# Kernel tuning notes

Hardware: AMD Instinct MI355X
Metric: run time of the kernel (lower is better)

## Reference

```python
import jax, jax.numpy as jnp
import numpy as np

B, T, D_MODEL, N_HEAD, D_C = 2, 2048, 2048, 16, 512
D_HEAD = D_MODEL // N_HEAD          # 128
D_ROPE = D_C // N_HEAD              # 32 (rope projections are split into heads too)


def setup_inputs() -> dict:
    key = jax.random.key(0)
    ks = jax.random.split(key, 16)
    s = 0.02
    # weights stored as [in, out] (transpose of torch Linear.weight)
    return {
        "x":     jax.random.normal(ks[0], (B, T, D_MODEL), jnp.float32),
        "W_DKV": jax.random.normal(ks[1], (D_MODEL, D_C), jnp.float32) * s,
        "b_DKV": jnp.zeros((D_C,), jnp.float32),
        "W_UK":  jax.random.normal(ks[2], (D_C, D_MODEL), jnp.float32) * s,
        "b_UK":  jnp.zeros((D_MODEL,), jnp.float32),
        "W_UV":  jax.random.normal(ks[3], (D_C, D_MODEL), jnp.float32) * s,
        "b_UV":  jnp.zeros((D_MODEL,), jnp.float32),
        "W_DQ":  jax.random.normal(ks[4], (D_MODEL, D_C), jnp.float32) * s,
        "b_DQ":  jnp.zeros((D_C,), jnp.float32),
        "W_UQ":  jax.random.normal(ks[5], (D_C, D_MODEL), jnp.float32) * s,
        "b_UQ":  jnp.zeros((D_MODEL,), jnp.float32),
        "W_QR":  jax.random.normal(ks[6], (D_C, D_C), jnp.float32) * s,
        "b_QR":  jnp.zeros((D_C,), jnp.float32),
        "W_KR":  jax.random.normal(ks[7], (D_MODEL, D_C), jnp.float32) * s,
        "b_KR":  jnp.zeros((D_C,), jnp.float32),
    }


def _rope(x):
    # x: [B, H, T, d]; matches torch RoPE: split-even/odd then concat halves
    t, d = x.shape[2], x.shape[-1]
    freqs = 10000.0 ** (-(jnp.arange(0, d, 2, dtype=jnp.float32) / d))  # [d/2]
    theta = jnp.arange(t, dtype=jnp.float32)[:, None] * freqs[None, :]  # [T, d/2]
    cos, sin = jnp.cos(theta), jnp.sin(theta)
    x1, x2 = x[..., ::2], x[..., 1::2]
    return jnp.concatenate([x1 * cos - x2 * sin, x1 * sin + x2 * cos], axis=-1)


def _heads(x):
    b, t, _ = x.shape
    return x.reshape(b, t, N_HEAD, -1).transpose(0, 2, 1, 3)  # [B,H,T,dh]


def reference(x, W_DKV, b_DKV, W_UK, b_UK, W_UV, b_UV, W_DQ, b_DQ,
              W_UQ, b_UQ, W_QR, b_QR, W_KR, b_KR):
    b, t, _ = x.shape
    c_kv = x @ W_DKV + b_DKV                 # [B,T,d_c]
    k_content = _heads(c_kv @ W_UK + b_UK)   # [B,H,T,d_head]
    v = _heads(c_kv @ W_UV + b_UV)           # [B,H,T,d_head]
    c_q = x @ W_DQ + b_DQ
    q_content = _heads(c_q @ W_UQ + b_UQ)    # [B,H,T,d_head]
    q_rope = _rope(_heads(c_q @ W_QR + b_QR))  # [B,H,T,d_rope]
    k_rope = _rope(_heads(x @ W_KR + b_KR))    # [B,H,T,d_rope]
    Q = jnp.concatenate([q_content, q_rope], axis=-1)  # [B,H,T,d_head+d_rope]
    K = jnp.concatenate([k_content, k_rope], axis=-1)
    scale = 1.0 / jnp.sqrt(jnp.float32(Q.shape[-1]))
    scores = jnp.einsum("bhqd,bhkd->bhqk", Q, K) * scale
    probs = jax.nn.softmax(scores, axis=-1)
    out = jnp.einsum("bhqk,bhkd->bhqd", probs, v)
    return out.transpose(0, 2, 1, 3).reshape(b, t, -1)
```

## Files before the change

kernel.cpp:

```cpp
#include <hip/hip_runtime.h>
#include <hip/hip_bf16.h>
#include <cstdint>
#include <cstddef>

typedef __attribute__((ext_vector_type(8)))  short bf16x8;
typedef __attribute__((ext_vector_type(4)))  float f32x4;
typedef __attribute__((ext_vector_type(16))) float f32x16;
typedef __attribute__((ext_vector_type(4)))  int   i32x4;

#define DEVINL __device__ __forceinline__

#define ATT_SCALE 0.07905694150420949f
#define QSCALE    (0.07905694150420949f * 1.4426950408889634f)

DEVINL unsigned short f2bf(float f) {
  unsigned int u = __float_as_uint(f);
  u += 0x7fff + ((u >> 16) & 1);
  return (unsigned short)(u >> 16);
}

DEVINL int cvtpk(float lo, float hi) {
  int r;
  asm("v_cvt_pk_bf16_f32 %0, %1, %2" : "=v"(r) : "v"(lo), "v"(hi));
  return r;
}

DEVINL void stage16(const unsigned short* __restrict__ g, unsigned short* lds_u, int lane) {
  (void)lane;
  __builtin_amdgcn_global_load_lds((const __attribute__((address_space(1))) void*)g,
                                   (__attribute__((address_space(3))) void*)lds_u, 16, 0, 0);
}

__global__ void k_cvt_x(const float* __restrict__ x, unsigned short* __restrict__ o, int n) {
  int i = (blockIdx.x * blockDim.x + threadIdx.x) * 4;
  if (i >= n) return;
  float4 v = *reinterpret_cast<const float4*>(x + i);
  ushort4 r;
  r.x = f2bf(v.x); r.y = f2bf(v.y); r.z = f2bf(v.z); r.w = f2bf(v.w);
  *reinterpret_cast<ushort4*>(o + i) = r;
}

struct TwArgs { const float* W[7]; unsigned short* D[7]; };
__global__ void k_tw_all(TwArgs a) {
  __shared__ float t[32][33];
  const int bid = blockIdx.x;
  int w, K, N, bx, by;
  if (bid < 3072)      { w = bid >> 10; int r = bid & 1023; K = 2048; N = 512;  bx = r & 15; by = r >> 4; }
  else if (bid < 6144) { int r = bid - 3072; w = 3 + (r >> 10); r &= 1023; K = 512; N = 2048; bx = r & 63; by = r >> 6; }
  else                 { int r = bid - 6144; w = 6; K = 512; N = 512; bx = r & 15; by = r >> 4; }
  const float* W = a.W[w];
  unsigned short* D = a.D[w];
  const int n0 = bx * 32, k0 = by * 32;
  const int tx = threadIdx.x, ty = threadIdx.y;
#pragma unroll
  for (int j = 0; j < 4; j++)
    t[ty + j * 8][tx] = W[(size_t)(k0 + ty + j * 8) * N + n0 + tx];
  __syncthreads();
#pragma unroll
  for (int j = 0; j < 4; j++)
    D[(size_t)(n0 + ty + j * 8) * K + k0 + tx] = f2bf(t[tx][ty + j * 8]);
}

DEVINL size_t koff(int bh, int t, int d) {
  const int it = t >> 6, t6 = t & 63;
  const int kvt = t6 >> 5, lanelo = t6 & 31;
  const int ks = d >> 4, hi = (d >> 3) & 1, e = d & 7;
  return ((size_t)bh * 32 + it) * 10240 + (size_t)(kvt * 10 + ks) * 512 + (hi * 32 + lanelo) * 8 + e;
}
DEVINL size_t voff(int bh, int t, int dv) {
  const int it = t >> 6, t6 = t & 63;
  const int ks = t6 >> 4, hi = (t6 >> 3) & 1, e = t6 & 7;
  const int dvt = dv >> 5, lanelo = dv & 31;
  return ((size_t)bh * 32 + it) * 8192 + (size_t)(dvt * 4 + ks) * 512 + (hi * 32 + lanelo) * 8 + e;
}

__global__ __launch_bounds__(256) void k_gemm1(const unsigned short* __restrict__ A,
                                               const unsigned short* __restrict__ BT,
                                               const float* __restrict__ bias0,
                                               const float* __restrict__ bias1,
                                               const float* __restrict__ bias2,
                                               unsigned short* __restrict__ o0,
                                               unsigned short* __restrict__ o1,
                                               float* __restrict__ o2) {
  __shared__ unsigned short sA[128 * 64];
  __shared__ unsigned short sB[128 * 64];
  const int K = 2048;
  const int tid = threadIdx.x;
  const int lane = tid & 63, wid = tid >> 6;
  const int wr = wid >> 1, wc = wid & 1;
  const int row0 = blockIdx.y * 128, col0 = blockIdx.x * 128;
  const int lc = lane & 15, lg = lane >> 4;
  const int srow = lane >> 3, scol = (lane & 7) * 8;

  f32x4 acc[4][4];
#pragma unroll
  for (int m = 0; m < 4; m++)
#pragma unroll
    for (int n = 0; n < 4; n++) acc[m][n] = f32x4{0.f, 0.f, 0.f, 0.f};

  for (int k0 = 0; k0 < K; k0 += 64) {
#pragma unroll
    for (int i = 0; i < 4; i++) {
      const int chunk = wid * 4 + i;
      const int r = chunk * 8 + srow;
      stage16(A + (size_t)(row0 + r) * K + k0 + scol, sA + chunk * 512, lane);
      stage16(BT + (size_t)(col0 + r) * K + k0 + scol, sB + chunk * 512, lane);
    }
    asm volatile("s_waitcnt vmcnt(0)" ::: "memory");
    __syncthreads();
#pragma unroll
    for (int ks = 0; ks < 2; ks++) {
      bf16x8 af[4], bfr[4];
#pragma unroll
      for (int m = 0; m < 4; m++)
        af[m] = *reinterpret_cast<const bf16x8*>(sA + (wr * 64 + m * 16 + lc) * 64 + ks * 32 + lg * 8);
#pragma unroll
      for (int n = 0; n < 4; n++)
        bfr[n] = *reinterpret_cast<const bf16x8*>(sB + (wc * 64 + n * 16 + lc) * 64 + ks * 32 + lg * 8);
#pragma unroll
      for (int m = 0; m < 4; m++)
#pragma unroll
        for (int n = 0; n < 4; n++)
          acc[m][n] = __builtin_amdgcn_mfma_f32_16x16x32_bf16(af[m], bfr[n], acc[m][n], 0, 0, 0);
    }
    __syncthreads();
  }

  const int lr = lg * 4;
#pragma unroll
  for (int m = 0; m < 4; m++)
#pragma unroll
    for (int n = 0; n < 4; n++) {
      const int col = col0 + wc * 64 + n * 16 + lc;
      const float bv = (col < 512) ? bias0[col] : (col < 1024) ? bias1[col - 512] : bias2[col - 1024];
#pragma unroll
      for (int r = 0; r < 4; r++) {
        const int row = row0 + wr * 64 + m * 16 + lr + r;
        const float v = acc[m][n][r] + bv;
        if (col < 512)        o0[(size_t)row * 512 + col] = f2bf(v);
        else if (col < 1024)  o1[(size_t)row * 512 + col - 512] = f2bf(v);
        else                  o2[(size_t)row * 512 + col - 1024] = v;
      }
    }
}

__global__ __launch_bounds__(256) void k_gemm2(const unsigned short* __restrict__ ckv,
                                               const unsigned short* __restrict__ cq,
                                               const unsigned short* __restrict__ WT2,
                                               const unsigned short* __restrict__ WT3,
                                               const float* __restrict__ bUK,
                                               const float* __restrict__ bUV,
                                               const float* __restrict__ bUQ,
                                               const float* __restrict__ bQR,
                                               unsigned short* __restrict__ Kfb,
                                               unsigned short* __restrict__ Vfb,
                                               unsigned short* __restrict__ Qbuf,
                                               float* __restrict__ qrp) {
  __shared__ unsigned short sA[128 * 64];
  __shared__ unsigned short sB[128 * 64];
  const int K = 512;
  const bool m11 = blockIdx.x < 32;
  const unsigned short* A  = m11 ? ckv : cq;
  const unsigned short* BT = m11 ? WT2 : WT3;
  const int tid = threadIdx.x;
  const int lane = tid & 63, wid = tid >> 6;
  const int wr = wid >> 1, wc = wid & 1;
  const int row0 = blockIdx.y * 128;
  const int col0 = (m11 ? blockIdx.x : (blockIdx.x - 32)) * 128;
  const int lc = lane & 15, lg = lane >> 4;
  const int srow = lane >> 3, scol = (lane & 7) * 8;

  f32x4 acc[4][4];
#pragma unroll
  for (int m = 0; m < 4; m++)
#pragma unroll
    for (int n = 0; n < 4; n++) acc[m][n] = f32x4{0.f, 0.f, 0.f, 0.f};

  for (int k0 = 0; k0 < K; k0 += 64) {
#pragma unroll
    for (int i = 0; i < 4; i++) {
      const int chunk = wid * 4 + i;
      const int r = chunk * 8 + srow;
      stage16(A + (size_t)(row0 + r) * K + k0 + scol, sA + chunk * 512, lane);
      stage16(BT + (size_t)(col0 + r) * K + k0 + scol, sB + chunk * 512, lane);
    }
    asm volatile("s_waitcnt vmcnt(0)" ::: "memory");
    __syncthreads();
#pragma unroll
    for (int ks = 0; ks < 2; ks++) {
      bf16x8 af[4], bfr[4];
#pragma unroll
      for (int m = 0; m < 4; m++)
        af[m] = *reinterpret_cast<const bf16x8*>(sA + (wr * 64 + m * 16 + lc) * 64 + ks * 32 + lg * 8);
#pragma unroll
      for (int n = 0; n < 4; n++)
        bfr[n] = *reinterpret_cast<const bf16x8*>(sB + (wc * 64 + n * 16 + lc) * 64 + ks * 32 + lg * 8);
#pragma unroll
      for (int m = 0; m < 4; m++)
#pragma unroll
        for (int n = 0; n < 4; n++)
          acc[m][n] = __builtin_amdgcn_mfma_f32_16x16x32_bf16(af[m], bfr[n], acc[m][n], 0, 0, 0);
    }
    __syncthreads();
  }

  const int lr = lg * 4;
#pragma unroll
  for (int m = 0; m < 4; m++)
#pragma unroll
    for (int n = 0; n < 4; n++) {
      const int col = col0 + wc * 64 + n * 16 + lc;
      float bv;
      if (m11) bv = (col < 2048) ? bUK[col] : bUV[col - 2048];
      else     bv = (col < 2048) ? bUQ[col] : bQR[col - 2048];
#pragma unroll
      for (int r = 0; r < 4; r++) {
        const int row = row0 + wr * 64 + m * 16 + lr + r;
        const float v = acc[m][n][r] + bv;
        const int b = row >> 11, t = row & 2047;
        if (m11) {
          if (col < 2048) {
            const int h = col >> 7, d = col & 127;
            Kfb[koff(b * 16 + h, t, d)] = f2bf(v);
          } else {
            const int c = col - 2048, h = c >> 7, dv = c & 127;
            Vfb[voff(b * 16 + h, t, dv)] = f2bf(v);
          }
        } else {
          if (col < 2048) {
            const int h = col >> 7, d = col & 127;
            Qbuf[((size_t)(b * 16 + h) * 2048 + t) * 160 + d] = f2bf(v * QSCALE);
          } else {
            qrp[(size_t)row * 512 + col - 2048] = v;
          }
        }
      }
    }
}

__global__ void k_rope(const float* __restrict__ qpre, const float* __restrict__ kpre,
                       unsigned short* __restrict__ Qb, unsigned short* __restrict__ Kf) {
  const int idx = blockIdx.x * blockDim.x + threadIdx.x;
  const int which = idx >> 20;
  const int e = idx & 1048575;
  const int i = e & 15, h = (e >> 4) & 15, row = e >> 8;
  const int t = row & 2047, b = row >> 11;
  const float* pre = which ? kpre : qpre;
  const float x1 = pre[(size_t)row * 512 + h * 32 + 2 * i];
  const float x2 = pre[(size_t)row * 512 + h * 32 + 2 * i + 1];
  const float f = exp2f(-(float)i * (13.287712379549449f / 16.f));
  const float th = (float)t * f;
  float sv, cv;
  sincosf(th, &sv, &cv);
  const float o1 = x1 * cv - x2 * sv, o2 = x1 * sv + x2 * cv;
  if (which == 0) {
    const size_t base = ((size_t)(b * 16 + h) * 2048 + t) * 160 + 128;
    Qb[base + i]      = f2bf(o1 * QSCALE);
    Qb[base + 16 + i] = f2bf(o2 * QSCALE);
  } else {
    Kf[koff(b * 16 + h, t, 128 + i)] = f2bf(o1);
    Kf[koff(b * 16 + h, t, 144 + i)] = f2bf(o2);
  }
}

DEVINL float vmax32(const f32x16& a, const f32x16& b) {
  float t[16];
#pragma unroll
  for (int j = 0; j < 16; j++) t[j] = fmaxf(a[j], b[j]);
#pragma unroll
  for (int s = 8; s >= 1; s >>= 1)
#pragma unroll
    for (int j = 0; j < s; j++) t[j] = fmaxf(t[j], t[j + s]);
  return t[0];
}

DEVINL void loadV(const unsigned short* __restrict__ Vt, bf16x8 v[16], int lane) {
#pragma unroll
  for (int f = 0; f < 16; f++)
    v[f] = *reinterpret_cast<const bf16x8*>(Vt + (size_t)f * 512 + lane * 8);
}

DEVINL void subiter(const unsigned short* __restrict__ sKb, const bf16x8 qf[10],
                    const bf16x8 vfr[16], f32x16 o[4], float& mrun, float& lrun,
                    int lane, int hi) {
  f32x16 s0 = {}, s1 = {};
  __builtin_amdgcn_s_setprio(1);
#pragma unroll
  for (int ks = 0; ks < 10; ks++) {
    bf16x8 kf0 = *reinterpret_cast<const bf16x8*>(sKb + (size_t)ks * 512 + lane * 8);
    s0 = __builtin_amdgcn_mfma_f32_32x32x16_bf16(kf0, qf[ks], s0, 0, 0, 0);
    bf16x8 kf1 = *reinterpret_cast<const bf16x8*>(sKb + (size_t)(10 + ks) * 512 + lane * 8);
    s1 = __builtin_amdgcn_mfma_f32_32x32x16_bf16(kf1, qf[ks], s1, 0, 0, 0);
  }
  __builtin_amdgcn_s_setprio(0);

  float mx = vmax32(s0, s1);
  mx = fmaxf(mx, __shfl_xor(mx, 32));

  if (__any(mx > mrun + 8.f)) {
    const float mn = fmaxf(mrun, mx);
    const float corr = exp2f(mrun - mn);
    lrun *= corr;
#pragma unroll
    for (int d = 0; d < 4; d++)
#pragma unroll
      for (int r = 0; r < 16; r++) o[d][r] *= corr;
    mrun = mn;
  }

  float pe0[16], pe1[16];
#pragma unroll
  for (int r = 0; r < 16; r++) pe0[r] = exp2f(s0[r] - mrun);
#pragma unroll
  for (int r = 0; r < 16; r++) pe1[r] = exp2f(s1[r] - mrun);
  float a[16];
#pragma unroll
  for (int j = 0; j < 8; j++) {
    a[j]     = pe0[2 * j] + pe0[2 * j + 1];
    a[8 + j] = pe1[2 * j] + pe1[2 * j + 1];
  }
#pragma unroll
  for (int s = 8; s >= 1; s >>= 1)
#pragma unroll
    for (int j = 0; j < s; j++) a[j] += a[j + s];
  float rs = a[0];
  rs += __shfl_xor(rs, 32);
  lrun += rs;

  int W0[8], W1[8], S0w[8], S1w[8];
#pragma unroll
  for (int j = 0; j < 8; j++) {
    W0[j] = cvtpk(pe0[2 * j], pe0[2 * j + 1]);
    W1[j] = cvtpk(pe1[2 * j], pe1[2 * j + 1]);
  }
#pragma unroll
  for (int j = 0; j < 8; j++) {
    S0w[j] = __shfl_xor(W0[j], 32);
    S1w[j] = __shfl_xor(W1[j], 32);
  }
  bf16x8 pa[4];
  {
    i32x4 w0 = hi ? i32x4{S0w[2], S0w[3], W0[2], W0[3]} : i32x4{W0[0], W0[1], S0w[0], S0w[1]};
    i32x4 w1 = hi ? i32x4{S0w[6], S0w[7], W0[6], W0[7]} : i32x4{W0[4], W0[5], S0w[4], S0w[5]};
    i32x4 w2 = hi ? i32x4{S1w[2], S1w[3], W1[2], W1[3]} : i32x4{W1[0], W1[1], S1w[0], S1w[1]};
    i32x4 w3 = hi ? i32x4{S1w[6], S1w[7], W1[6], W1[7]} : i32x4{W1[4], W1[5], S1w[4], S1w[5]};
    pa[0] = __builtin_bit_cast(bf16x8, w0);
    pa[1] = __builtin_bit_cast(bf16x8, w1);
    pa[2] = __builtin_bit_cast(bf16x8, w2);
    pa[3] = __builtin_bit_cast(bf16x8, w3);
  }

  __builtin_amdgcn_s_setprio(1);
#pragma unroll
  for (int ks = 0; ks < 4; ks++) {
    o[0] = __builtin_amdgcn_mfma_f32_32x32x16_bf16(vfr[ks],      pa[ks], o[0], 0, 0, 0);
    o[1] = __builtin_amdgcn_mfma_f32_32x32x16_bf16(vfr[4 + ks],  pa[ks], o[1], 0, 0, 0);
    o[2] = __builtin_amdgcn_mfma_f32_32x32x16_bf16(vfr[8 + ks],  pa[ks], o[2], 0, 0, 0);
    o[3] = __builtin_amdgcn_mfma_f32_32x32x16_bf16(vfr[12 + ks], pa[ks], o[3], 0, 0, 0);
  }
  __builtin_amdgcn_s_setprio(0);
}

__global__ __launch_bounds__(256, 2) void k_attn(const unsigned short* __restrict__ Qb,
                                                 const unsigned short* __restrict__ Kf,
                                                 const unsigned short* __restrict__ Vf,
                                                 float* __restrict__ out) {
  __shared__ unsigned short sK[4][10240];
  const int lane = threadIdx.x & 63, wid = threadIdx.x >> 6;
  const int lanelo = lane & 31, hi = lane >> 5;

  const int L = blockIdx.x;
  const int xcd = L & 7, w = L >> 3;
  const int bh = xcd * 4 + (w & 3);
  const int qblk = w >> 2;
  const int b = bh >> 4, h = bh & 15;
  const int q0 = qblk * 128 + wid * 32;

  const unsigned short* Qh = Qb + (size_t)bh * 2048 * 160;
  const unsigned short* Kh = Kf + (size_t)bh * 32 * 10240;
  const unsigned short* Vh = Vf + (size_t)bh * 32 * 8192;

  bf16x8 qf[10];
#pragma unroll
  for (int ks = 0; ks < 10; ks++)
    qf[ks] = *reinterpret_cast<const bf16x8*>(Qh + (size_t)(q0 + lanelo) * 160 + ks * 16 + hi * 8);

#pragma unroll
  for (int i = 0; i < 10; i++) {
    const int chunk = wid * 10 + i;
    stage16(Kh + (size_t)chunk * 512 + lane * 8, &sK[0][0] + chunk * 512, lane);
  }

  f32x16 o[4] = {};
  float mrun = -1e30f, lrun = 0.f;

  asm volatile("s_waitcnt vmcnt(0)" ::: "memory");
  __syncthreads();

  for (int p = 0; p < 16; p++) {
    const int base = (p & 1) * 2;
    bf16x8 vA[16];
    loadV(Vh + (size_t)(2 * p) * 8192, vA, lane);
    if (p < 15) {
      const unsigned short* src = Kh + (size_t)(2 * p + 2) * 10240;
      unsigned short* dst = &sK[base ^ 2][0];
#pragma unroll
      for (int i = 0; i < 10; i++) {
        const int chunk = wid * 10 + i;
        stage16(src + (size_t)chunk * 512 + lane * 8, dst + chunk * 512, lane);
      }
    }
    subiter(&sK[base][0], qf, vA, o, mrun, lrun, lane, hi);
    bf16x8 vB[16];
    loadV(Vh + (size_t)(2 * p + 1) * 8192, vB, lane);
    subiter(&sK[base + 1][0], qf, vB, o, mrun, lrun, lane, hi);

    asm volatile("s_waitcnt vmcnt(0)" ::: "memory");
    __syncthreads();
  }

  const float inv = 1.f / lrun;
  float* sO = reinterpret_cast<float*>(&sK[0][0]) + wid * 1152;
#pragma unroll
  for (int dvt = 0; dvt < 4; dvt++) {
    __syncthreads();
#pragma unroll
    for (int r = 0; r < 16; r++) {
      const int dvl = (r & 3) + 8 * (r >> 2) + 4 * hi;
      sO[lanelo * 36 + dvl] = o[dvt][r] * inv;
    }
    __syncthreads();
#pragma unroll
    for (int p = 0; p < 4; p++) {
      const int q = p * 8 + (lane >> 3), c = (lane & 7) * 4;
      float4 v = *reinterpret_cast<const float4*>(sO + q * 36 + c);
      *reinterpret_cast<float4*>(out + ((size_t)b * 2048 + q0 + q) * 2048 + h * 128 + dvt * 32 + c) = v;
    }
  }
}

extern "C" void kernel_launch(void* const* d_in, const int* in_sizes, int n_in,
                              void* d_out, int out_size, void* d_ws, size_t ws_size,
                              hipStream_t stream) {
  (void)in_sizes; (void)n_in; (void)out_size;
  const float* x     = (const float*)d_in[0];
  const float* W_DKV = (const float*)d_in[1];
  const float* b_DKV = (const float*)d_in[2];
  const float* W_UK  = (const float*)d_in[3];
  const float* b_UK  = (const float*)d_in[4];
  const float* W_UV  = (const float*)d_in[5];
  const float* b_UV  = (const float*)d_in[6];
  const float* W_DQ  = (const float*)d_in[7];
  const float* b_DQ  = (const float*)d_in[8];
  const float* W_UQ  = (const float*)d_in[9];
  const float* b_UQ  = (const float*)d_in[10];
  const float* W_QR  = (const float*)d_in[11];
  const float* b_QR  = (const float*)d_in[12];
  const float* W_KR  = (const float*)d_in[13];
  const float* b_KR  = (const float*)d_in[14];
  float* out = (float*)d_out;

  char* ws = (char*)d_ws;
  unsigned short* xb     = (unsigned short*)(ws + 0);
  unsigned short* WTcat1 = (unsigned short*)(ws + 16777216);
  unsigned short* WTcat2 = (unsigned short*)(ws + 23068672);
  unsigned short* WTcat3 = (unsigned short*)(ws + 27262976);
  unsigned short* ckv    = (unsigned short*)(ws + 29884416);
  unsigned short* cq     = (unsigned short*)(ws + 34078720);
  unsigned short* Qbuf   = (unsigned short*)(ws + 38273024);
  unsigned short* Kfb    = (unsigned short*)(ws + 59244544);
  unsigned short* Vfb    = (unsigned short*)(ws + 80216064);
  float*          qrp    = (float*)(ws + 96993280);
  float*          krp    = (float*)(ws + 105381888);
  if (ws_size < 113770496) return;

  k_cvt_x<<<8192, 256, 0, stream>>>(x, xb, 8388608);

  TwArgs ta;
  ta.W[0] = W_DKV; ta.D[0] = WTcat1;
  ta.W[1] = W_DQ;  ta.D[1] = WTcat1 + (size_t)512 * 2048;
  ta.W[2] = W_KR;  ta.D[2] = WTcat1 + (size_t)1024 * 2048;
  ta.W[3] = W_UK;  ta.D[3] = WTcat2;
  ta.W[4] = W_UV;  ta.D[4] = WTcat2 + (size_t)2048 * 512;
  ta.W[5] = W_UQ;  ta.D[5] = WTcat3;
  ta.W[6] = W_QR;  ta.D[6] = WTcat3 + (size_t)2048 * 512;
  k_tw_all<<<6400, dim3(32, 8), 0, stream>>>(ta);

  k_gemm1<<<dim3(12, 32), 256, 0, stream>>>(xb, WTcat1, b_DKV, b_DQ, b_KR, ckv, cq, krp);
  k_gemm2<<<dim3(52, 32), 256, 0, stream>>>(ckv, cq, WTcat2, WTcat3,
                                            b_UK, b_UV, b_UQ, b_QR,
                                            Kfb, Vfb, Qbuf, qrp);

  k_rope<<<8192, 256, 0, stream>>>(qrp, krp, Qbuf, Kfb);
  k_attn<<<512, 256, 0, stream>>>(Qbuf, Kfb, Vfb, out);
}
```

Before: 370.7 us.

## Fuse prep kernels, retile gemm1 to 128x64, specialize gemm2 epilogue, single-tile attention loop

Merges the x bf16 conversion and the weight transpose into one prep launch. Halves the gemm1 column tile so twice as many blocks run (768 vs 384), which fills the CUs better at the cost of more A-tile reloads. Specializes the gemm2 epilogue per output region so each branch uses a uniform segment and packed or strided stores. Restructures attention to one K tile per iteration with two LDS buffers instead of four, dropping setprio hints, which lowers LDS use but adds more barriers.

```diff
diff --git a/kernel.cpp b/kernel.cpp
--- a/kernel.cpp
+++ b/kernel.cpp
@@ -10,8 +10,7 @@
 
 #define DEVINL __device__ __forceinline__
 
-#define ATT_SCALE 0.07905694150420949f
-#define QSCALE    (0.07905694150420949f * 1.4426950408889634f)
+#define QSCALE (0.07905694150420949f * 1.4426950408889634f)
 
 DEVINL unsigned short f2bf(float f) {
   unsigned int u = __float_as_uint(f);
@@ -25,33 +24,32 @@
   return r;
 }
 
-DEVINL void stage16(const unsigned short* __restrict__ g, unsigned short* lds_u, int lane) {
-  (void)lane;
+DEVINL void stage16(const unsigned short* __restrict__ g, unsigned short* lds_u) {
   __builtin_amdgcn_global_load_lds((const __attribute__((address_space(1))) void*)g,
                                    (__attribute__((address_space(3))) void*)lds_u, 16, 0, 0);
 }
 
-__global__ void k_cvt_x(const float* __restrict__ x, unsigned short* __restrict__ o, int n) {
-  int i = (blockIdx.x * blockDim.x + threadIdx.x) * 4;
-  if (i >= n) return;
-  float4 v = *reinterpret_cast<const float4*>(x + i);
-  ushort4 r;
-  r.x = f2bf(v.x); r.y = f2bf(v.y); r.z = f2bf(v.z); r.w = f2bf(v.w);
-  *reinterpret_cast<ushort4*>(o + i) = r;
-}
-
 struct TwArgs { const float* W[7]; unsigned short* D[7]; };
-__global__ void k_tw_all(TwArgs a) {
+__global__ void k_prep(const float* __restrict__ x, unsigned short* __restrict__ xb, TwArgs a) {
   __shared__ float t[32][33];
-  const int bid = blockIdx.x;
+  const int bid = blockIdx.x, tid = threadIdx.x;
+  if (bid < 8192) {
+    const int i = (bid * 256 + tid) * 4;
+    float4 v = *reinterpret_cast<const float4*>(x + i);
+    ushort4 r;
+    r.x = f2bf(v.x); r.y = f2bf(v.y); r.z = f2bf(v.z); r.w = f2bf(v.w);
+    *reinterpret_cast<ushort4*>(xb + i) = r;
+    return;
+  }
+  const int tb = bid - 8192;
   int w, K, N, bx, by;
-  if (bid < 3072)      { w = bid >> 10; int r = bid & 1023; K = 2048; N = 512;  bx = r & 15; by = r >> 4; }
-  else if (bid < 6144) { int r = bid - 3072; w = 3 + (r >> 10); r &= 1023; K = 512; N = 2048; bx = r & 63; by = r >> 6; }
-  else                 { int r = bid - 6144; w = 6; K = 512; N = 512; bx = r & 15; by = r >> 4; }
+  if (tb < 3072)      { w = tb >> 10; int r = tb & 1023; K = 2048; N = 512;  bx = r & 15; by = r >> 4; }
+  else if (tb < 6144) { int r = tb - 3072; w = 3 + (r >> 10); r &= 1023; K = 512; N = 2048; bx = r & 63; by = r >> 6; }
+  else                 { int r = tb - 6144; w = 6; K = 512; N = 512; bx = r & 15; by = r >> 4; }
   const float* W = a.W[w];
   unsigned short* D = a.D[w];
   const int n0 = bx * 32, k0 = by * 32;
-  const int tx = threadIdx.x, ty = threadIdx.y;
+  const int tx = tid & 31, ty = tid >> 5;
 #pragma unroll
   for (int j = 0; j < 4; j++)
     t[ty + j * 8][tx] = W[(size_t)(k0 + ty + j * 8) * N + n0 + tx];
@@ -83,42 +81,44 @@
                                                unsigned short* __restrict__ o1,
                                                float* __restrict__ o2) {
   __shared__ unsigned short sA[128 * 64];
-  __shared__ unsigned short sB[128 * 64];
+  __shared__ unsigned short sB[64 * 64];
   const int K = 2048;
   const int tid = threadIdx.x;
   const int lane = tid & 63, wid = tid >> 6;
-  const int wr = wid >> 1, wc = wid & 1;
-  const int row0 = blockIdx.y * 128, col0 = blockIdx.x * 128;
+  const int row0 = blockIdx.y * 128, col0 = blockIdx.x * 64;
   const int lc = lane & 15, lg = lane >> 4;
   const int srow = lane >> 3, scol = (lane & 7) * 8;
 
-  f32x4 acc[4][4];
-#pragma unroll
-  for (int m = 0; m < 4; m++)
+  f32x4 acc[2][4];
+#pragma unroll
+  for (int m = 0; m < 2; m++)
 #pragma unroll
     for (int n = 0; n < 4; n++) acc[m][n] = f32x4{0.f, 0.f, 0.f, 0.f};
 
   for (int k0 = 0; k0 < K; k0 += 64) {
 #pragma unroll
-    for (int i = 0; i < 4; i++) {
-      const int chunk = wid * 4 + i;
-      const int r = chunk * 8 + srow;
-      stage16(A + (size_t)(row0 + r) * K + k0 + scol, sA + chunk * 512, lane);
-      stage16(BT + (size_t)(col0 + r) * K + k0 + scol, sB + chunk * 512, lane);
+    for (int i = 0; i < 6; i++) {
+      const int chunk = wid * 6 + i;
+      if (chunk < 16) {
+        stage16(A + (size_t)(row0 + chunk * 8 + srow) * K + k0 + scol, sA + chunk * 512);
+      } else {
+        const int c = chunk - 16;
+        stage16(BT + (size_t)(col0 + c * 8 + srow) * K + k0 + scol, sB + c * 512);
+      }
     }
     asm volatile("s_waitcnt vmcnt(0)" ::: "memory");
     __syncthreads();
 #pragma unroll
     for (int ks = 0; ks < 2; ks++) {
-      bf16x8 af[4], bfr[4];
-#pragma unroll
-      for (int m = 0; m < 4; m++)
-        af[m] = *reinterpret_cast<const bf16x8*>(sA + (wr * 64 + m * 16 + lc) * 64 + ks * 32 + lg * 8);
+      bf16x8 af[2], bfr[4];
+#pragma unroll
+      for (int m = 0; m < 2; m++)
+        af[m] = *reinterpret_cast<const bf16x8*>(sA + (wid * 32 + m * 16 + lc) * 64 + ks * 32 + lg * 8);
 #pragma unroll
       for (int n = 0; n < 4; n++)
-        bfr[n] = *reinterpret_cast<const bf16x8*>(sB + (wc * 64 + n * 16 + lc) * 64 + ks * 32 + lg * 8);
-#pragma unroll
-      for (int m = 0; m < 4; m++)
+        bfr[n] = *reinterpret_cast<const bf16x8*>(sB + (n * 16 + lc) * 64 + ks * 32 + lg * 8);
+#pragma unroll
+      for (int m = 0; m < 2; m++)
 #pragma unroll
         for (int n = 0; n < 4; n++)
           acc[m][n] = __builtin_amdgcn_mfma_f32_16x16x32_bf16(af[m], bfr[n], acc[m][n], 0, 0, 0);
@@ -126,20 +126,23 @@
     __syncthreads();
   }
 
+  const int seg = col0 >> 9;
+  const int cofs = col0 - seg * 512;
+  const float* bp = (seg == 0) ? bias0 : (seg == 1) ? bias1 : bias2;
   const int lr = lg * 4;
 #pragma unroll
-  for (int m = 0; m < 4; m++)
+  for (int m = 0; m < 2; m++)
 #pragma unroll
     for (int n = 0; n < 4; n++) {
-      const int col = col0 + wc * 64 + n * 16 + lc;
-      const float bv = (col < 512) ? bias0[col] : (col < 1024) ? bias1[col - 512] : bias2[col - 1024];
+      const int c = cofs + n * 16 + lc;
+      const float bv = bp[c];
 #pragma unroll
       for (int r = 0; r < 4; r++) {
-        const int row = row0 + wr * 64 + m * 16 + lr + r;
+        const int row = row0 + wid * 32 + m * 16 + lr + r;
         const float v = acc[m][n][r] + bv;
-        if (col < 512)        o0[(size_t)row * 512 + col] = f2bf(v);
-        else if (col < 1024)  o1[(size_t)row * 512 + col - 512] = f2bf(v);
-        else                  o2[(size_t)row * 512 + col - 1024] = v;
+        if (seg == 0)      o0[(size_t)row * 512 + c] = f2bf(v);
+        else if (seg == 1) o1[(size_t)row * 512 + c] = f2bf(v);
+        else               o2[(size_t)row * 512 + c] = v;
       }
     }
 }
@@ -159,14 +162,15 @@
   __shared__ unsigned short sA[128 * 64];
   __shared__ unsigned short sB[128 * 64];
   const int K = 512;
-  const bool m11 = blockIdx.x < 32;
+  const int bx = blockIdx.x;
+  const bool m11 = bx < 32;
   const unsigned short* A  = m11 ? ckv : cq;
   const unsigned short* BT = m11 ? WT2 : WT3;
   const int tid = threadIdx.x;
   const int lane = tid & 63, wid = tid >> 6;
   const int wr = wid >> 1, wc = wid & 1;
   const int row0 = blockIdx.y * 128;
-  const int col0 = (m11 ? blockIdx.x : (blockIdx.x - 32)) * 128;
+  const int col0 = (m11 ? bx : (bx - 32)) * 128;
   const int lc = lane & 15, lg = lane >> 4;
   const int srow = lane >> 3, scol = (lane & 7) * 8;
 
@@ -181,8 +185,8 @@
     for (int i = 0; i < 4; i++) {
       const int chunk = wid * 4 + i;
       const int r = chunk * 8 + srow;
-      stage16(A + (size_t)(row0 + r) * K + k0 + scol, sA + chunk * 512, lane);
-      stage16(BT + (size_t)(col0 + r) * K + k0 + scol, sB + chunk * 512, lane);
+      stage16(A + (size_t)(row0 + r) * K + k0 + scol, sA + chunk * 512);
+      stage16(BT + (size_t)(col0 + r) * K + k0 + scol, sB + chunk * 512);
     }
     asm volatile("s_waitcnt vmcnt(0)" ::: "memory");
     __syncthreads();
@@ -205,37 +209,71 @@
   }
 
   const int lr = lg * 4;
-#pragma unroll
-  for (int m = 0; m < 4; m++)
-#pragma unroll
-    for (int n = 0; n < 4; n++) {
-      const int col = col0 + wc * 64 + n * 16 + lc;
-      float bv;
-      if (m11) bv = (col < 2048) ? bUK[col] : bUV[col - 2048];
-      else     bv = (col < 2048) ? bUQ[col] : bQR[col - 2048];
-#pragma unroll
-      for (int r = 0; r < 4; r++) {
-        const int row = row0 + wr * 64 + m * 16 + lr + r;
-        const float v = acc[m][n][r] + bv;
-        const int b = row >> 11, t = row & 2047;
-        if (m11) {
-          if (col < 2048) {
-            const int h = col >> 7, d = col & 127;
-            Kfb[koff(b * 16 + h, t, d)] = f2bf(v);
-          } else {
-            const int c = col - 2048, h = c >> 7, dv = c & 127;
-            Vfb[voff(b * 16 + h, t, dv)] = f2bf(v);
-          }
-        } else {
-          if (col < 2048) {
-            const int h = col >> 7, d = col & 127;
-            Qbuf[((size_t)(b * 16 + h) * 2048 + t) * 160 + d] = f2bf(v * QSCALE);
-          } else {
-            qrp[(size_t)row * 512 + col - 2048] = v;
-          }
+  const int b = blockIdx.y >> 4;
+  const int t0 = (blockIdx.y & 15) * 128;
+
+  if (bx < 16) {
+    const int bh = b * 16 + bx;
+#pragma unroll
+    for (int m = 0; m < 4; m++)
+#pragma unroll
+      for (int n = 0; n < 4; n++) {
+        const int d = wc * 64 + n * 16 + lc;
+        const float bv = bUK[bx * 128 + d];
+        const int t = t0 + wr * 64 + m * 16 + lr;
+        const size_t ko = koff(bh, t, d);
+#pragma unroll
+        for (int r = 0; r < 4; r++)
+          Kfb[ko + 8 * r] = f2bf(acc[m][n][r] + bv);
+      }
+  } else if (bx < 32) {
+    const int h = bx - 16, bh = b * 16 + h;
+#pragma unroll
+    for (int m = 0; m < 4; m++)
+#pragma unroll
+      for (int n = 0; n < 4; n++) {
+        const int dv = wc * 64 + n * 16 + lc;
+        const float bv = bUV[h * 128 + dv];
+        const int t = t0 + wr * 64 + m * 16 + lr;
+        const size_t vo = voff(bh, t, dv);
+        ushort4 pk;
+        pk.x = f2bf(acc[m][n][0] + bv);
+        pk.y = f2bf(acc[m][n][1] + bv);
+        pk.z = f2bf(acc[m][n][2] + bv);
+        pk.w = f2bf(acc[m][n][3] + bv);
+        *reinterpret_cast<ushort4*>(Vfb + vo) = pk;
+      }
+  } else if (bx < 48) {
+    const int h = bx - 32;
+#pragma unroll
+    for (int m = 0; m < 4; m++)
+#pragma unroll
+      for (int n = 0; n < 4; n++) {
+        const int d = wc * 64 + n * 16 + lc;
+        const float bv = bUQ[h * 128 + d];
+        const int t = t0 + wr * 64 + m * 16 + lr;
+        size_t qo = ((size_t)(b * 16 + h) * 2048 + t) * 160 + d;
+#pragma unroll
+        for (int r = 0; r < 4; r++) {
+          Qbuf[qo] = f2bf((acc[m][n][r] + bv) * QSCALE);
+          qo += 160;
         }
       }
-    }
+  } else {
+    const int c0 = (bx - 48) * 128;
+#pragma unroll
+    for (int m = 0; m < 4; m++)
+#pragma unroll
+      for (int n = 0; n < 4; n++) {
+        const int c = c0 + wc * 64 + n * 16 + lc;
+        const float bv = bQR[c];
+#pragma unroll
+        for (int r = 0; r < 4; r++) {
+          const int row = blockIdx.y * 128 + wr * 64 + m * 16 + lr + r;
+          qrp[(size_t)row * 512 + c] = acc[m][n][r] + bv;
+        }
+      }
+  }
 }
 
 __global__ void k_rope(const float* __restrict__ qpre, const float* __restrict__ kpre,
@@ -263,109 +301,11 @@
   }
 }
 
-DEVINL float vmax32(const f32x16& a, const f32x16& b) {
-  float t[16];
-#pragma unroll
-  for (int j = 0; j < 16; j++) t[j] = fmaxf(a[j], b[j]);
-#pragma unroll
-  for (int s = 8; s >= 1; s >>= 1)
-#pragma unroll
-    for (int j = 0; j < s; j++) t[j] = fmaxf(t[j], t[j + s]);
-  return t[0];
-}
-
-DEVINL void loadV(const unsigned short* __restrict__ Vt, bf16x8 v[16], int lane) {
-#pragma unroll
-  for (int f = 0; f < 16; f++)
-    v[f] = *reinterpret_cast<const bf16x8*>(Vt + (size_t)f * 512 + lane * 8);
-}
-
-DEVINL void subiter(const unsigned short* __restrict__ sKb, const bf16x8 qf[10],
-                    const bf16x8 vfr[16], f32x16 o[4], float& mrun, float& lrun,
-                    int lane, int hi) {
-  f32x16 s0 = {}, s1 = {};
-  __builtin_amdgcn_s_setprio(1);
-#pragma unroll
-  for (int ks = 0; ks < 10; ks++) {
-    bf16x8 kf0 = *reinterpret_cast<const bf16x8*>(sKb + (size_t)ks * 512 + lane * 8);
-    s0 = __builtin_amdgcn_mfma_f32_32x32x16_bf16(kf0, qf[ks], s0, 0, 0, 0);
-    bf16x8 kf1 = *reinterpret_cast<const bf16x8*>(sKb + (size_t)(10 + ks) * 512 + lane * 8);
-    s1 = __builtin_amdgcn_mfma_f32_32x32x16_bf16(kf1, qf[ks], s1, 0, 0, 0);
-  }
-  __builtin_amdgcn_s_setprio(0);
-
-  float mx = vmax32(s0, s1);
-  mx = fmaxf(mx, __shfl_xor(mx, 32));
-
-  if (__any(mx > mrun + 8.f)) {
-    const float mn = fmaxf(mrun, mx);
-    const float corr = exp2f(mrun - mn);
-    lrun *= corr;
-#pragma unroll
-    for (int d = 0; d < 4; d++)
-#pragma unroll
-      for (int r = 0; r < 16; r++) o[d][r] *= corr;
-    mrun = mn;
-  }
-
-  float pe0[16], pe1[16];
-#pragma unroll
-  for (int r = 0; r < 16; r++) pe0[r] = exp2f(s0[r] - mrun);
-#pragma unroll
-  for (int r = 0; r < 16; r++) pe1[r] = exp2f(s1[r] - mrun);
-  float a[16];
-#pragma unroll
-  for (int j = 0; j < 8; j++) {
-    a[j]     = pe0[2 * j] + pe0[2 * j + 1];
-    a[8 + j] = pe1[2 * j] + pe1[2 * j + 1];
-  }
-#pragma unroll
-  for (int s = 8; s >= 1; s >>= 1)
-#pragma unroll
-    for (int j = 0; j < s; j++) a[j] += a[j + s];
-  float rs = a[0];
-  rs += __shfl_xor(rs, 32);
-  lrun += rs;
-
-  int W0[8], W1[8], S0w[8], S1w[8];
-#pragma unroll
-  for (int j = 0; j < 8; j++) {
-    W0[j] = cvtpk(pe0[2 * j], pe0[2 * j + 1]);
-    W1[j] = cvtpk(pe1[2 * j], pe1[2 * j + 1]);
-  }
-#pragma unroll
-  for (int j = 0; j < 8; j++) {
-    S0w[j] = __shfl_xor(W0[j], 32);
-    S1w[j] = __shfl_xor(W1[j], 32);
-  }
-  bf16x8 pa[4];
-  {
-    i32x4 w0 = hi ? i32x4{S0w[2], S0w[3], W0[2], W0[3]} : i32x4{W0[0], W0[1], S0w[0], S0w[1]};
-    i32x4 w1 = hi ? i32x4{S0w[6], S0w[7], W0[6], W0[7]} : i32x4{W0[4], W0[5], S0w[4], S0w[5]};
-    i32x4 w2 = hi ? i32x4{S1w[2], S1w[3], W1[2], W1[3]} : i32x4{W1[0], W1[1], S1w[0], S1w[1]};
-    i32x4 w3 = hi ? i32x4{S1w[6], S1w[7], W1[6], W1[7]} : i32x4{W1[4], W1[5], S1w[4], S1w[5]};
-    pa[0] = __builtin_bit_cast(bf16x8, w0);
-    pa[1] = __builtin_bit_cast(bf16x8, w1);
-    pa[2] = __builtin_bit_cast(bf16x8, w2);
-    pa[3] = __builtin_bit_cast(bf16x8, w3);
-  }
-
-  __builtin_amdgcn_s_setprio(1);
-#pragma unroll
-  for (int ks = 0; ks < 4; ks++) {
-    o[0] = __builtin_amdgcn_mfma_f32_32x32x16_bf16(vfr[ks],      pa[ks], o[0], 0, 0, 0);
-    o[1] = __builtin_amdgcn_mfma_f32_32x32x16_bf16(vfr[4 + ks],  pa[ks], o[1], 0, 0, 0);
-    o[2] = __builtin_amdgcn_mfma_f32_32x32x16_bf16(vfr[8 + ks],  pa[ks], o[2], 0, 0, 0);
-    o[3] = __builtin_amdgcn_mfma_f32_32x32x16_bf16(vfr[12 + ks], pa[ks], o[3], 0, 0, 0);
-  }
-  __builtin_amdgcn_s_setprio(0);
-}
-
 __global__ __launch_bounds__(256, 2) void k_attn(const unsigned short* __restrict__ Qb,
                                                  const unsigned short* __restrict__ Kf,
                                                  const unsigned short* __restrict__ Vf,
                                                  float* __restrict__ out) {
-  __shared__ unsigned short sK[4][10240];
+  __shared__ unsigned short sK[2][10240];
   const int lane = threadIdx.x & 63, wid = threadIdx.x >> 6;
   const int lanelo = lane & 31, hi = lane >> 5;
 
@@ -386,9 +326,9 @@
     qf[ks] = *reinterpret_cast<const bf16x8*>(Qh + (size_t)(q0 + lanelo) * 160 + ks * 16 + hi * 8);
 
 #pragma unroll
-  for (int i = 0; i < 10; i++) {
-    const int chunk = wid * 10 + i;
-    stage16(Kh + (size_t)chunk * 512 + lane * 8, &sK[0][0] + chunk * 512, lane);
+  for (int i = 0; i < 5; i++) {
+    const int chunk = wid * 5 + i;
+    stage16(Kh + (size_t)chunk * 512 + lane * 8, &sK[0][0] + chunk * 512);
   }
 
   f32x16 o[4] = {};
@@ -397,26 +337,105 @@
   asm volatile("s_waitcnt vmcnt(0)" ::: "memory");
   __syncthreads();
 
-  for (int p = 0; p < 16; p++) {
-    const int base = (p & 1) * 2;
-    bf16x8 vA[16];
-    loadV(Vh + (size_t)(2 * p) * 8192, vA, lane);
-    if (p < 15) {
-      const unsigned short* src = Kh + (size_t)(2 * p + 2) * 10240;
-      unsigned short* dst = &sK[base ^ 2][0];
-#pragma unroll
-      for (int i = 0; i < 10; i++) {
-        const int chunk = wid * 10 + i;
-        stage16(src + (size_t)chunk * 512 + lane * 8, dst + chunk * 512, lane);
-      }
-    }
-    subiter(&sK[base][0], qf, vA, o, mrun, lrun, lane, hi);
-    bf16x8 vB[16];
-    loadV(Vh + (size_t)(2 * p + 1) * 8192, vB, lane);
-    subiter(&sK[base + 1][0], qf, vB, o, mrun, lrun, lane, hi);
+  int buf = 0;
+  for (int it = 0; it < 32; it++) {
+    bf16x8 vf[16];
+    {
+      const unsigned short* Vt = Vh + (size_t)it * 8192;
+#pragma unroll
+      for (int f = 0; f < 16; f++)
+        vf[f] = *reinterpret_cast<const bf16x8*>(Vt + (size_t)f * 512 + lane * 8);
+    }
+    if (it < 31) {
+      const unsigned short* src = Kh + (size_t)(it + 1) * 10240;
+      unsigned short* dst = &sK[buf ^ 1][0];
+#pragma unroll
+      for (int i = 0; i < 5; i++) {
+        const int chunk = wid * 5 + i;
+        stage16(src + (size_t)chunk * 512 + lane * 8, dst + chunk * 512);
+      }
+    }
+    f32x16 s0 = {}, s1 = {};
+    const unsigned short* sKb = &sK[buf][0];
+#pragma unroll
+    for (int ks = 0; ks < 10; ks++) {
+      bf16x8 kf0 = *reinterpret_cast<const bf16x8*>(sKb + (size_t)ks * 512 + lane * 8);
+      s0 = __builtin_amdgcn_mfma_f32_32x32x16_bf16(kf0, qf[ks], s0, 0, 0, 0);
+      bf16x8 kf1 = *reinterpret_cast<const bf16x8*>(sKb + (size_t)(10 + ks) * 512 + lane * 8);
+      s1 = __builtin_amdgcn_mfma_f32_32x32x16_bf16(kf1, qf[ks], s1, 0, 0, 0);
+    }
+
+    float tm[16];
+#pragma unroll
+    for (int j = 0; j < 16; j++) tm[j] = fmaxf(s0[j], s1[j]);
+#pragma unroll
+    for (int s = 8; s >= 1; s >>= 1)
+#pragma unroll
+      for (int j = 0; j < s; j++) tm[j] = fmaxf(tm[j], tm[j + s]);
+    float mx = fmaxf(tm[0], __shfl_xor(tm[0], 32));
+
+    if (__any(mx > mrun + 8.f)) {
+      const float mn = fmaxf(mrun, mx);
+      const float corr = exp2f(mrun - mn);
+      lrun *= corr;
+#pragma unroll
+      for (int d = 0; d < 4; d++)
+#pragma unroll
+        for (int r = 0; r < 16; r++) o[d][r] *= corr;
+      mrun = mn;
+    }
+
+    float pe0[16], pe1[16];
+#pragma unroll
+    for (int r = 0; r < 16; r++) pe0[r] = exp2f(s0[r] - mrun);
+#pragma unroll
+    for (int r = 0; r < 16; r++) pe1[r] = exp2f(s1[r] - mrun);
+    float ta[16];
+#pragma unroll
+    for (int j = 0; j < 8; j++) {
+      ta[j]     = pe0[2 * j] + pe0[2 * j + 1];
+      ta[8 + j] = pe1[2 * j] + pe1[2 * j + 1];
+    }
+#pragma unroll
+    for (int s = 8; s >= 1; s >>= 1)
+#pragma unroll
+      for (int j = 0; j < s; j++) ta[j] += ta[j + s];
+    lrun += ta[0] + __shfl_xor(ta[0], 32);
+
+    int W0[8], W1[8], S0w[8], S1w[8];
+#pragma unroll
+    for (int j = 0; j < 8; j++) {
+      W0[j] = cvtpk(pe0[2 * j], pe0[2 * j + 1]);
+      W1[j] = cvtpk(pe1[2 * j], pe1[2 * j + 1]);
+    }
+#pragma unroll
+    for (int j = 0; j < 8; j++) {
+      S0w[j] = __shfl_xor(W0[j], 32);
+      S1w[j] = __shfl_xor(W1[j], 32);
+    }
+    bf16x8 pa[4];
+    {
+      i32x4 w0 = hi ? i32x4{S0w[2], S0w[3], W0[2], W0[3]} : i32x4{W0[0], W0[1], S0w[0], S0w[1]};
+      i32x4 w1 = hi ? i32x4{S0w[6], S0w[7], W0[6], W0[7]} : i32x4{W0[4], W0[5], S0w[4], S0w[5]};
+      i32x4 w2 = hi ? i32x4{S1w[2], S1w[3], W1[2], W1[3]} : i32x4{W1[0], W1[1], S1w[0], S1w[1]};
+      i32x4 w3 = hi ? i32x4{S1w[6], S1w[7], W1[6], W1[7]} : i32x4{W1[4], W1[5], S1w[4], S1w[5]};
+      pa[0] = __builtin_bit_cast(bf16x8, w0);
+      pa[1] = __builtin_bit_cast(bf16x8, w1);
+      pa[2] = __builtin_bit_cast(bf16x8, w2);
+      pa[3] = __builtin_bit_cast(bf16x8, w3);
+    }
+
+#pragma unroll
+    for (int ks = 0; ks < 4; ks++) {
+      o[0] = __builtin_amdgcn_mfma_f32_32x32x16_bf16(vf[ks],      pa[ks], o[0], 0, 0, 0);
+      o[1] = __builtin_amdgcn_mfma_f32_32x32x16_bf16(vf[4 + ks],  pa[ks], o[1], 0, 0, 0);
+      o[2] = __builtin_amdgcn_mfma_f32_32x32x16_bf16(vf[8 + ks],  pa[ks], o[2], 0, 0, 0);
+      o[3] = __builtin_amdgcn_mfma_f32_32x32x16_bf16(vf[12 + ks], pa[ks], o[3], 0, 0, 0);
+    }
 
     asm volatile("s_waitcnt vmcnt(0)" ::: "memory");
     __syncthreads();
+    buf ^= 1;
   }
 
   const float inv = 1.f / lrun;
@@ -474,8 +493,6 @@
   float*          krp    = (float*)(ws + 105381888);
   if (ws_size < 113770496) return;
 
-  k_cvt_x<<<8192, 256, 0, stream>>>(x, xb, 8388608);
-
   TwArgs ta;
   ta.W[0] = W_DKV; ta.D[0] = WTcat1;
   ta.W[1] = W_DQ;  ta.D[1] = WTcat1 + (size_t)512 * 2048;
@@ -484,9 +501,9 @@
   ta.W[4] = W_UV;  ta.D[4] = WTcat2 + (size_t)2048 * 512;
   ta.W[5] = W_UQ;  ta.D[5] = WTcat3;
   ta.W[6] = W_QR;  ta.D[6] = WTcat3 + (size_t)2048 * 512;
-  k_tw_all<<<6400, dim3(32, 8), 0, stream>>>(ta);
-
-  k_gemm1<<<dim3(12, 32), 256, 0, stream>>>(xb, WTcat1, b_DKV, b_DQ, b_KR, ckv, cq, krp);
+  k_prep<<<14592, 256, 0, stream>>>(x, xb, ta);
+
+  k_gemm1<<<dim3(24, 32), 256, 0, stream>>>(xb, WTcat1, b_DKV, b_DQ, b_KR, ckv, cq, krp);
   k_gemm2<<<dim3(52, 32), 256, 0, stream>>>(ckv, cq, WTcat2, WTcat3,
                                             b_UK, b_UV, b_UQ, b_QR,
                                             Kfb, Vfb, Qbuf, qrp);
```

Measured after the change: 340.4 us. 8.2% less time.
